# Optimization experiments

Hardware: AMD Instinct MI355X
Metric: run time of the kernel (lower is better)

The kernel has to match this reference:

```python
import jax, jax.numpy as jnp
import numpy as np

B, T, IN = 4, 1024, 172
D, H, FF, L, NCLS = 512, 8, 2048, 8, 1296
HD = D // H
EPS = 1e-5


def setup_inputs() -> dict:
    key = jax.random.key(0)
    ks = jax.random.split(key, 16)
    rn = lambda k, s, sc=0.02: jax.random.normal(k, s, jnp.float32) * sc
    return {
        "poses": jax.random.normal(ks[0], (B, T, IN), jnp.float32),
        "pose_w": rn(ks[1], (D, IN)), "pose_b": jnp.zeros((D,), jnp.float32),
        "in_w": rn(ks[2], (L, 3 * D, D)), "in_b": jnp.zeros((L, 3 * D), jnp.float32),
        "out_w": rn(ks[3], (L, D, D)), "out_b": jnp.zeros((L, D), jnp.float32),
        "ln1_g": jnp.ones((L, D), jnp.float32), "ln1_b": jnp.zeros((L, D), jnp.float32),
        "ffn_w1": rn(ks[4], (L, FF, D)), "ffn_b1": jnp.zeros((L, FF), jnp.float32),
        "ffn_w2": rn(ks[5], (L, D, FF)), "ffn_b2": jnp.zeros((L, D), jnp.float32),
        "ln2_g": jnp.ones((L, D), jnp.float32), "ln2_b": jnp.zeros((L, D), jnp.float32),
        "tcn1_w": rn(ks[6], (512, D, 5)), "tcn1_b": jnp.zeros((512,), jnp.float32),
        "tcn2_w": rn(ks[7], (D, 512, 5)), "tcn2_b": jnp.zeros((D,), jnp.float32),
        "fc1_w": rn(ks[8], (128, D)), "fc1_b": jnp.zeros((128,), jnp.float32),
        "fc2_w": rn(ks[9], (NCLS, 128)), "fc2_b": jnp.zeros((NCLS,), jnp.float32),
    }


def _pos_enc(seq_len, d):
    # PositionalEncoding1D: interleaved sin/cos per frequency pair
    inv_freq = 1.0 / (10000.0 ** (jnp.arange(0, d, 2, dtype=jnp.float32) / d))
    ang = jnp.arange(seq_len, dtype=jnp.float32)[:, None] * inv_freq  # [T, d/2]
    return jnp.stack([jnp.sin(ang), jnp.cos(ang)], axis=-1).reshape(seq_len, d)


def _ln(x, g, b):
    m = x.mean(-1, keepdims=True)
    v = jnp.var(x, axis=-1, keepdims=True)
    return (x - m) * jax.lax.rsqrt(v + EPS) * g + b


def _encoder_layer(x, iw, ib, ow, ob, g1, b1, w1, c1, w2, c2, g2, b2):
    # post-norm TransformerEncoderLayer, eager (non-flash) attention
    Bc, Tc, _ = x.shape
    qkv = x @ iw.T + ib                       # [B,T,3D]
    q, k, v = jnp.split(qkv, 3, axis=-1)
    q = q.reshape(Bc, Tc, H, HD)
    k = k.reshape(Bc, Tc, H, HD)
    v = v.reshape(Bc, Tc, H, HD)
    scores = jnp.einsum('bqhd,bkhd->bhqk', q, k) / jnp.sqrt(jnp.float32(HD))
    attn = jax.nn.softmax(scores, axis=-1)    # explicit weights (need_weights=True)
    o = jnp.einsum('bhqk,bkhd->bqhd', attn, v).reshape(Bc, Tc, D)
    o = o @ ow.T + ob
    x = _ln(x + o, g1, b1)
    f = jax.nn.relu(x @ w1.T + c1) @ w2.T + c2
    return _ln(x + f, g2, b2)


def _conv1d(x, w, b):  # x [B,T,C_in], w [C_out,C_in,5], pad=2
    y = jax.lax.conv_general_dilated(
        x.transpose(0, 2, 1), w, window_strides=(1,), padding=((2, 2),),
        dimension_numbers=('NCH', 'OIH', 'NCH'))
    return y.transpose(0, 2, 1) + b


def _avgpool2(x):  # kernel=2 stride=2 along time
    Bc, Tc, C = x.shape
    return x.reshape(Bc, Tc // 2, 2, C).mean(axis=2)


def reference(poses, pose_w, pose_b, in_w, in_b, out_w, out_b, ln1_g, ln1_b,
              ffn_w1, ffn_b1, ffn_w2, ffn_b2, ln2_g, ln2_b,
              tcn1_w, tcn1_b, tcn2_w, tcn2_b, fc1_w, fc1_b, fc2_w, fc2_b):
    x = poses.reshape(poses.shape[0], poses.shape[1], -1) @ pose_w.T + pose_b
    x = x + _pos_enc(x.shape[1], D)[None]

    def run_stack(h, idx):
        for i in idx:
            h = _encoder_layer(h, in_w[i], in_b[i], out_w[i], out_b[i],
                               ln1_g[i], ln1_b[i], ffn_w1[i], ffn_b1[i],
                               ffn_w2[i], ffn_b2[i], ln2_g[i], ln2_b[i])
        return h

    h = run_stack(x, (0, 1))
    h = run_stack(h, (2, 3)) + h
    h = run_stack(h, (4, 5)) + h
    h = run_stack(h, (6, 7)) + h

    h = _avgpool2(h)                 # [B,T/2,D]
    h = _conv1d(h, tcn1_w, tcn1_b)   # [B,T/2,512]
    h = _avgpool2(h)                 # [B,T/4,512]
    h = _conv1d(h, tcn2_w, tcn2_b)   # [B,T/4,D]
    h = h @ fc1_w.T + fc1_b
    logits = h @ fc2_w.T + fc2_b     # [B,T/4,num_classes]
    return logits
```

## Files before the change

kernel.cpp:

```cpp
#include <hip/hip_runtime.h>
#include <hip/hip_bf16.h>

static constexpr int kB = 4;
static constexpr int kT = 1024;
static constexpr int kIn = 172;
static constexpr int kD = 512;
static constexpr int kH = 8;
static constexpr int kHD = 64;
static constexpr int kFF = 2048;
static constexpr int kNCLS = 1296;
static constexpr float kEps = 1e-5f;

typedef __attribute__((ext_vector_type(8))) short bf16x8_t;
typedef __attribute__((ext_vector_type(4))) float f32x4_t;
typedef __attribute__((ext_vector_type(8))) unsigned short u16x8_t;
typedef __attribute__((ext_vector_type(4))) unsigned short u16x4_t;

static __device__ __forceinline__ unsigned short f2bf(float f) {
  unsigned int u = __float_as_uint(f);
  unsigned int r = (u + 0x7fffu + ((u >> 16) & 1u)) >> 16;
  return (unsigned short)r;
}

__global__ void cvt_kernel(const float* __restrict__ src, ushort* __restrict__ dst, int n8)
{
  const int i = blockIdx.x * 256 + threadIdx.x;
  if (i >= n8) return;
  const float4 a = *(const float4*)&src[i * 8];
  const float4 b = *(const float4*)&src[i * 8 + 4];
  u16x8_t t;
  t[0] = f2bf(a.x); t[1] = f2bf(a.y); t[2] = f2bf(a.z); t[3] = f2bf(a.w);
  t[4] = f2bf(b.x); t[5] = f2bf(b.y); t[6] = f2bf(b.z); t[7] = f2bf(b.w);
  *(u16x8_t*)&dst[i * 8] = t;
}

template<int MR, int NR>
__global__ __launch_bounds__(256) void bgemm_kernel(
    const ushort* __restrict__ A, const ushort* __restrict__ W,
    const float* __restrict__ bias, const float* __restrict__ resid,
    float* __restrict__ C, ushort* __restrict__ Cb, int M, int N, int K, int doRelu)
{
  constexpr int BM = MR * 32, BN = NR * 32, BK = 32;
  constexpr int AI = BM / 64;
  constexpr int BI = BN / 64;
  __shared__ ushort As[BM * BK];
  __shared__ ushort Bs[BN * BK];

  const int tid = threadIdx.x;
  int bid = blockIdx.y * gridDim.x + blockIdx.x;
  const int nwg = gridDim.x * gridDim.y;
  if ((nwg & 7) == 0) bid = (bid & 7) * (nwg >> 3) + (bid >> 3);
  const int bm = (bid / gridDim.x) * BM, bn = (bid % gridDim.x) * BN;

  const int wv = tid >> 6, lane = tid & 63;
  const int lr = lane & 15, lg = lane >> 4;
  const int wr = wv >> 1, wc = wv & 1;

  const int arow0 = wv * (BM / 4);
  const int brow0 = wv * (BN / 4);
  const int lrow = lane >> 2;
  const int lchunk = (lane & 3) * 8;

  f32x4_t acc[MR][NR];
#pragma unroll
  for (int m = 0; m < MR; ++m)
#pragma unroll
    for (int n = 0; n < NR; ++n) acc[m][n] = (f32x4_t){0.f, 0.f, 0.f, 0.f};

  auto stage = [&](int k0) {
#pragma unroll
    for (int i = 0; i < AI; ++i) {
      const ushort* g = A + (size_t)(bm + arow0 + i * 16 + lrow) * K + k0 + lchunk;
      __builtin_amdgcn_global_load_lds(
          (const __attribute__((address_space(1))) void*)g,
          (__attribute__((address_space(3))) void*)&As[(arow0 + i * 16) * BK], 16, 0, 0);
    }
#pragma unroll
    for (int i = 0; i < BI; ++i) {
      const ushort* g = W + (size_t)(bn + brow0 + i * 16 + lrow) * K + k0 + lchunk;
      __builtin_amdgcn_global_load_lds(
          (const __attribute__((address_space(1))) void*)g,
          (__attribute__((address_space(3))) void*)&Bs[(brow0 + i * 16) * BK], 16, 0, 0);
    }
  };

  stage(0);
  const int nsteps = K >> 5;
  for (int s = 0; s < nsteps; ++s) {
    __syncthreads();
    bf16x8_t af[MR], bf[NR];
#pragma unroll
    for (int m = 0; m < MR; ++m)
      af[m] = *(const bf16x8_t*)&As[(wr * MR * 16 + m * 16 + lr) * BK + lg * 8];
#pragma unroll
    for (int n = 0; n < NR; ++n)
      bf[n] = *(const bf16x8_t*)&Bs[(wc * NR * 16 + n * 16 + lr) * BK + lg * 8];
#pragma unroll
    for (int n = 0; n < NR; ++n)
#pragma unroll
      for (int m = 0; m < MR; ++m)
        acc[m][n] = __builtin_amdgcn_mfma_f32_16x16x32_bf16(af[m], bf[n], acc[m][n], 0, 0, 0);
    __syncthreads();
    if (s + 1 < nsteps) stage((s + 1) << 5);
  }

#pragma unroll
  for (int m = 0; m < MR; ++m) {
#pragma unroll
    for (int v = 0; v < 4; ++v) {
      const int mm = bm + wr * MR * 16 + m * 16 + lg * 4 + v;
#pragma unroll
      for (int n = 0; n < NR; ++n) {
        const int nn = bn + wc * NR * 16 + n * 16 + lr;
        float val = acc[m][n][v] + bias[nn];
        if (doRelu) val = fmaxf(val, 0.f);
        if (resid) val += resid[(size_t)mm * N + nn];
        if (C)  C[(size_t)mm * N + nn] = val;
        if (Cb) Cb[(size_t)mm * N + nn] = f2bf(val);
      }
    }
  }
}

#define GBM 64
#define GBN 64
#define GBK 16
#define LDST 68

__global__ __launch_bounds__(256) void gemm_kernel(
    const float* __restrict__ A, const float* __restrict__ W,
    const float* __restrict__ bias, const float* __restrict__ resid,
    float* __restrict__ C, int M, int N, int K, int doRelu)
{
  __shared__ __align__(16) float As[GBK][LDST];
  __shared__ __align__(16) float Ws[GBK][LDST];
  const int tid = threadIdx.x;
  const int bm = blockIdx.y * GBM;
  const int bn = blockIdx.x * GBN;
  const int tx = tid & 15, ty = tid >> 4;
  const int li = tid >> 2;
  const int lk = (tid & 3) << 2;

  float acc[4][4];
#pragma unroll
  for (int i = 0; i < 4; ++i)
#pragma unroll
    for (int j = 0; j < 4; ++j) acc[i][j] = 0.f;

  for (int k0 = 0; k0 < K; k0 += GBK) {
    float4 av = make_float4(0.f, 0.f, 0.f, 0.f);
    float4 wv = make_float4(0.f, 0.f, 0.f, 0.f);
    {
      const int m = bm + li;
      if (m < M) {
        if (k0 + lk + 4 <= K) {
          av = *(const float4*)&A[(size_t)m * K + k0 + lk];
        } else {
          float t4[4] = {0.f, 0.f, 0.f, 0.f};
          for (int c = 0; c < 4; ++c) { int k = k0 + lk + c; if (k < K) t4[c] = A[(size_t)m * K + k]; }
          av = make_float4(t4[0], t4[1], t4[2], t4[3]);
        }
      }
      const int n = bn + li;
      if (n < N) {
        if (k0 + lk + 4 <= K) {
          wv = *(const float4*)&W[(size_t)n * K + k0 + lk];
        } else {
          float t4[4] = {0.f, 0.f, 0.f, 0.f};
          for (int c = 0; c < 4; ++c) { int k = k0 + lk + c; if (k < K) t4[c] = W[(size_t)n * K + k]; }
          wv = make_float4(t4[0], t4[1], t4[2], t4[3]);
        }
      }
    }
    __syncthreads();
    As[lk + 0][li] = av.x; As[lk + 1][li] = av.y; As[lk + 2][li] = av.z; As[lk + 3][li] = av.w;
    Ws[lk + 0][li] = wv.x; Ws[lk + 1][li] = wv.y; Ws[lk + 2][li] = wv.z; Ws[lk + 3][li] = wv.w;
    __syncthreads();
#pragma unroll
    for (int kk = 0; kk < GBK; ++kk) {
      const float4 a4 = *(const float4*)&As[kk][ty << 2];
      const float4 b4 = *(const float4*)&Ws[kk][tx << 2];
      const float a[4] = {a4.x, a4.y, a4.z, a4.w};
      const float b[4] = {b4.x, b4.y, b4.z, b4.w};
#pragma unroll
      for (int i = 0; i < 4; ++i)
#pragma unroll
        for (int j = 0; j < 4; ++j) acc[i][j] = fmaf(a[i], b[j], acc[i][j]);
    }
  }

#pragma unroll
  for (int i = 0; i < 4; ++i) {
    const int m = bm + (ty << 2) + i;
    if (m >= M) continue;
#pragma unroll
    for (int j = 0; j < 4; ++j) {
      const int n = bn + (tx << 2) + j;
      if (n >= N) continue;
      float v = acc[i][j] + bias[n];
      if (doRelu) v = fmaxf(v, 0.f);
      if (resid) v += resid[(size_t)m * N + n];
      C[(size_t)m * N + n] = v;
    }
  }
}

__global__ __launch_bounds__(256) void ln_kernel(
    float* __restrict__ X, ushort* __restrict__ Xb,
    const float* __restrict__ g, const float* __restrict__ bta,
    const float* Padd, float* Pout)
{
  const int row = blockIdx.x;
  const int tid = threadIdx.x;
  float* xr = X + (size_t)row * kD;
  const float x0 = xr[tid];
  const float x1 = xr[tid + 256];
  float s = x0 + x1;
  float q = x0 * x0 + x1 * x1;
#pragma unroll
  for (int off = 32; off > 0; off >>= 1) {
    s += __shfl_down(s, off);
    q += __shfl_down(q, off);
  }
  __shared__ float ss[4], qq[4];
  const int w = tid >> 6;
  if ((tid & 63) == 0) { ss[w] = s; qq[w] = q; }
  __syncthreads();
  const float S = ss[0] + ss[1] + ss[2] + ss[3];
  const float Q = qq[0] + qq[1] + qq[2] + qq[3];
  const float mean = S * (1.f / kD);
  const float var = Q * (1.f / kD) - mean * mean;
  const float inv = rsqrtf(var + kEps);
  float v0 = (x0 - mean) * inv * g[tid] + bta[tid];
  float v1 = (x1 - mean) * inv * g[tid + 256] + bta[tid + 256];
  if (Padd) {
    v0 += Padd[(size_t)row * kD + tid];
    v1 += Padd[(size_t)row * kD + tid + 256];
  }
  xr[tid] = v0; xr[tid + 256] = v1;
  ushort* xb = Xb + (size_t)row * kD;
  xb[tid] = f2bf(v0); xb[tid + 256] = f2bf(v1);
  if (Pout) {
    Pout[(size_t)row * kD + tid] = v0;
    Pout[(size_t)row * kD + tid + 256] = v1;
  }
}

#define KSTR 72
#define PSTR 74
__global__ __launch_bounds__(256) void attn_mfma_kernel(
    const ushort* __restrict__ qkv, ushort* __restrict__ O)
{
  const int b = blockIdx.z, h = blockIdx.y;
  const int q0 = blockIdx.x << 6;
  const int tid = threadIdx.x;
  const int wv = tid >> 6, lane = tid & 63;
  const int lr = lane & 15;
  const int lg = lane >> 4;

  __shared__ ushort Ks[64 * KSTR];
  __shared__ ushort Vt[64 * KSTR];
  __shared__ ushort Pl[4][16 * PSTR];

  bf16x8_t qa[2];
  {
    const ushort* qrow = qkv + ((size_t)(b * kT + q0 + wv * 16 + lr)) * (3 * kD) + h * kHD + lg * 8;
    qa[0] = *(const bf16x8_t*)qrow;
    qa[1] = *(const bf16x8_t*)(qrow + 32);
  }

  float m_[4], l_[4];
  f32x4_t oacc[4];
#pragma unroll
  for (int r = 0; r < 4; ++r) { m_[r] = -1e30f; l_[r] = 0.f; }
#pragma unroll
  for (int nb = 0; nb < 4; ++nb) oacc[nb] = (f32x4_t){0.f, 0.f, 0.f, 0.f};

  const int srow = tid >> 2;
  const int sd   = (tid & 3) << 4;
  const int vkp  = tid & 31;
  const int vdh  = tid >> 5;

  u16x8_t k0_, k1_, v0_, v1_;
  auto load_regs = [&](int kt) {
    const ushort* kr = qkv + ((size_t)(b * kT + (kt << 6) + srow)) * (3 * kD) + kD + h * kHD + sd;
    k0_ = *(const u16x8_t*)kr;
    k1_ = *(const u16x8_t*)(kr + 8);
    const ushort* vr = qkv + ((size_t)(b * kT + (kt << 6) + 2 * vkp)) * (3 * kD) + 2 * kD + h * kHD + vdh * 8;
    v0_ = *(const u16x8_t*)vr;
    v1_ = *(const u16x8_t*)(vr + 3 * kD);
  };

  load_regs(0);
  for (int kt = 0; kt < kT / 64; ++kt) {
    __syncthreads();
    {
      *(u16x8_t*)&Ks[srow * KSTR + sd]     = k0_;
      *(u16x8_t*)&Ks[srow * KSTR + sd + 8] = k1_;
#pragma unroll
      for (int e = 0; e < 8; ++e) {
        const unsigned int packv = (unsigned int)v0_[e] | ((unsigned int)v1_[e] << 16);
        *(unsigned int*)&Vt[(vdh * 8 + e) * KSTR + 2 * vkp] = packv;
      }
    }
    __syncthreads();
    if (kt + 1 < kT / 64) load_regs(kt + 1);

    f32x4_t s[4];
#pragma unroll
    for (int cc = 0; cc < 4; ++cc) {
      const ushort* kb = &Ks[(cc * 16 + lr) * KSTR + lg * 8];
      const bf16x8_t kf0 = *(const bf16x8_t*)kb;
      const bf16x8_t kf1 = *(const bf16x8_t*)(kb + 32);
      f32x4_t acc = (f32x4_t){0.f, 0.f, 0.f, 0.f};
      acc = __builtin_amdgcn_mfma_f32_16x16x32_bf16(qa[0], kf0, acc, 0, 0, 0);
      acc = __builtin_amdgcn_mfma_f32_16x16x32_bf16(qa[1], kf1, acc, 0, 0, 0);
#pragma unroll
      for (int r = 0; r < 4; ++r) acc[r] *= 0.125f;
      s[cc] = acc;
    }

#pragma unroll
    for (int r = 0; r < 4; ++r) {
      float mx = fmaxf(fmaxf(s[0][r], s[1][r]), fmaxf(s[2][r], s[3][r]));
      mx = fmaxf(mx, __shfl_xor(mx, 1));
      mx = fmaxf(mx, __shfl_xor(mx, 2));
      mx = fmaxf(mx, __shfl_xor(mx, 4));
      mx = fmaxf(mx, __shfl_xor(mx, 8));
      const float mnew = fmaxf(m_[r], mx);
      const float alpha = __expf(m_[r] - mnew);
      float sum = 0.f;
#pragma unroll
      for (int cc = 0; cc < 4; ++cc) {
        const float p = __expf(s[cc][r] - mnew);
        s[cc][r] = p;
        sum += p;
      }
      sum += __shfl_xor(sum, 1);
      sum += __shfl_xor(sum, 2);
      sum += __shfl_xor(sum, 4);
      sum += __shfl_xor(sum, 8);
      l_[r] = l_[r] * alpha + sum;
      m_[r] = mnew;
#pragma unroll
      for (int nb = 0; nb < 4; ++nb) oacc[nb][r] *= alpha;
#pragma unroll
      for (int cc = 0; cc < 4; ++cc)
        Pl[wv][(lg * 4 + r) * PSTR + cc * 16 + lr] = f2bf(s[cc][r]);
    }

    const bf16x8_t pa0 = *(const bf16x8_t*)&Pl[wv][lr * PSTR + lg * 8];
    const bf16x8_t pa1 = *(const bf16x8_t*)&Pl[wv][lr * PSTR + 32 + lg * 8];
#pragma unroll
    for (int nb = 0; nb < 4; ++nb) {
      const ushort* vb = &Vt[(nb * 16 + lr) * KSTR + lg * 8];
      const bf16x8_t vf0 = *(const bf16x8_t*)vb;
      const bf16x8_t vf1 = *(const bf16x8_t*)(vb + 32);
      oacc[nb] = __builtin_amdgcn_mfma_f32_16x16x32_bf16(pa0, vf0, oacc[nb], 0, 0, 0);
      oacc[nb] = __builtin_amdgcn_mfma_f32_16x16x32_bf16(pa1, vf1, oacc[nb], 0, 0, 0);
    }
  }

#pragma unroll
  for (int nb = 0; nb < 4; ++nb) {
#pragma unroll
    for (int r = 0; r < 4; ++r) {
      const int row = lg * 4 + r;
      const int col = nb * 16 + lr;
      O[((size_t)(b * kT + q0 + wv * 16 + row)) * kD + h * kHD + col] = f2bf(oacc[nb][r] / l_[r]);
    }
  }
}

__global__ __launch_bounds__(256) void posenc_kernel(float* __restrict__ X, ushort* __restrict__ Xb)
{
  const int bt = blockIdx.x;
  const int t = bt & (kT - 1);
  float* row = X + (size_t)bt * kD;
  ushort* rb = Xb + (size_t)bt * kD;
#pragma unroll
  for (int p = 0; p < 2; ++p) {
    const int d = threadIdx.x + p * 256;
    const int j = d >> 1;
    const float inv = expf(-(float)j * 0.03597789207803197f);
    const float ang = (float)t * inv;
    const float pe = (d & 1) ? cosf(ang) : sinf(ang);
    const float v = row[d] + pe;
    row[d] = v;
    rb[d] = f2bf(v);
  }
}

__global__ void im2col_pool_kernel(const float* __restrict__ X, ushort* __restrict__ X5,
                                   int Tt, int n4)
{
  const int idx = blockIdx.x * 256 + threadIdx.x;
  if (idx >= n4) return;
  const int ci4 = idx & 127;
  int r = idx >> 7;
  const int tap = r % 5; r /= 5;
  const int t = r % Tt;
  const int b = r / Tt;
  const int ts = t + tap - 2;
  u16x4_t o = (u16x4_t){0, 0, 0, 0};
  if (ts >= 0 && ts < Tt) {
    const float* p = X + ((size_t)(b * 2 * Tt + 2 * ts)) * kD + ci4 * 4;
    const float4 x0 = *(const float4*)p;
    const float4 x1 = *(const float4*)(p + kD);
    o[0] = f2bf(0.5f * (x0.x + x1.x)); o[1] = f2bf(0.5f * (x0.y + x1.y));
    o[2] = f2bf(0.5f * (x0.z + x1.z)); o[3] = f2bf(0.5f * (x0.w + x1.w));
  }
  *(u16x4_t*)&X5[((size_t)(b * Tt + t)) * 2560 + tap * kD + ci4 * 4] = o;
}

__global__ void convw_t_kernel(const float* __restrict__ w, ushort* __restrict__ Wt)
{
  const int idx = blockIdx.x * 256 + threadIdx.x;
  if (idx >= 512 * 512 * 5) return;
  const int ci = idx & 511;
  int r = idx >> 9;
  const int tap = r % 5;
  const int co = r / 5;
  Wt[(size_t)co * 2560 + tap * 512 + ci] = f2bf(w[(size_t)co * 2560 + ci * 5 + tap]);
}

extern "C" void kernel_launch(void* const* d_in, const int* in_sizes, int n_in,
                              void* d_out, int out_size, void* d_ws, size_t ws_size,
                              hipStream_t stream)
{
  (void)in_sizes; (void)n_in; (void)out_size;
  const float* poses  = (const float*)d_in[0];
  const float* pose_w = (const float*)d_in[1];
  const float* pose_b = (const float*)d_in[2];
  const float* in_w   = (const float*)d_in[3];
  const float* in_b   = (const float*)d_in[4];
  const float* out_w  = (const float*)d_in[5];
  const float* out_b  = (const float*)d_in[6];
  const float* ln1_g  = (const float*)d_in[7];
  const float* ln1_b  = (const float*)d_in[8];
  const float* ffn_w1 = (const float*)d_in[9];
  const float* ffn_b1 = (const float*)d_in[10];
  const float* ffn_w2 = (const float*)d_in[11];
  const float* ffn_b2 = (const float*)d_in[12];
  const float* ln2_g  = (const float*)d_in[13];
  const float* ln2_b  = (const float*)d_in[14];
  const float* tcn1_w = (const float*)d_in[15];
  const float* tcn1_b = (const float*)d_in[16];
  const float* tcn2_w = (const float*)d_in[17];
  const float* tcn2_b = (const float*)d_in[18];
  const float* fc1_w  = (const float*)d_in[19];
  const float* fc1_b  = (const float*)d_in[20];
  const float* fc2_w  = (const float*)d_in[21];
  const float* fc2_b  = (const float*)d_in[22];

  char* base = (char*)d_ws;
  float*  A    = (float*)(base);
  float*  Y    = (float*)(base + 8388608);
  float*  P    = (float*)(base + 16777216);
  ushort* Abf  = (ushort*)(base + 25165824);
  ushort* QKV  = (ushort*)(base + 29360128);
  ushort* Ybf  = QKV;
  ushort* X5   = QKV;
  ushort* MID  = (ushort*)(base + 41943040);
  ushort* ATTb = MID;
  ushort* CW   = MID;
  ushort* Wbf  = (ushort*)(base + 58720256);

  const size_t nWq = (size_t)3 * kD * kD;
  const size_t nWo = (size_t)kD * kD;
  const size_t nW1 = (size_t)kFF * kD;
  const size_t nW2 = (size_t)kD * kFF;
  const size_t nWl = nWq + nWo + nW1 + nW2;
  const bool fullW = ws_size >= (size_t)58720256 + nWl * 8 * 2;

  const int M = kB * kT;
  dim3 blk(256);
  auto cvt = [&](const float* s, ushort* d, size_t n) {
    cvt_kernel<<<(int)((n / 8 + 255) / 256), blk, 0, stream>>>(s, d, (int)(n / 8));
  };

  if (fullW) {
    cvt(in_w,   Wbf,                        nWq * 8);
    cvt(out_w,  Wbf + nWq * 8,              nWo * 8);
    cvt(ffn_w1, Wbf + nWq * 8 + nWo * 8,    nW1 * 8);
    cvt(ffn_w2, Wbf + (nWq + nWo + nW1) * 8, nW2 * 8);
  }

  gemm_kernel<<<dim3(kD / GBN, M / GBM), blk, 0, stream>>>(poses, pose_w, pose_b, nullptr, A, M, kD, kIn, 0);
  posenc_kernel<<<M, blk, 0, stream>>>(A, Abf);

  for (int l = 0; l < 8; ++l) {
    const ushort *Wq, *Wo, *W1, *W2;
    if (fullW) {
      Wq = Wbf + (size_t)l * nWq;
      Wo = Wbf + nWq * 8 + (size_t)l * nWo;
      W1 = Wbf + nWq * 8 + nWo * 8 + (size_t)l * nW1;
      W2 = Wbf + (nWq + nWo + nW1) * 8 + (size_t)l * nW2;
    } else {
      cvt(in_w   + (size_t)l * nWq, Wbf, nWq);
      cvt(out_w  + (size_t)l * nWo, Wbf + nWq, nWo);
      cvt(ffn_w1 + (size_t)l * nW1, Wbf + nWq + nWo, nW1);
      cvt(ffn_w2 + (size_t)l * nW2, Wbf + nWq + nWo + nW1, nW2);
      Wq = Wbf; Wo = Wbf + nWq; W1 = Wbf + nWq + nWo; W2 = Wbf + nWq + nWo + nW1;
    }

    bgemm_kernel<4, 4><<<dim3(3 * kD / 128, M / 128), blk, 0, stream>>>(
        Abf, Wq, in_b + (size_t)l * 3 * kD, nullptr, nullptr, QKV, M, 3 * kD, kD, 0);
    attn_mfma_kernel<<<dim3(kT / 64, kH, kB), blk, 0, stream>>>(QKV, ATTb);
    bgemm_kernel<4, 2><<<dim3(kD / 64, M / 128), blk, 0, stream>>>(
        ATTb, Wo, out_b + (size_t)l * kD, A, Y, nullptr, M, kD, kD, 0);
    ln_kernel<<<M, blk, 0, stream>>>(Y, Ybf, ln1_g + (size_t)l * kD, ln1_b + (size_t)l * kD,
                                     nullptr, nullptr);
    bgemm_kernel<4, 4><<<dim3(kFF / 128, M / 128), blk, 0, stream>>>(
        Ybf, W1, ffn_b1 + (size_t)l * kFF, nullptr, nullptr, MID, M, kFF, kD, 1);
    bgemm_kernel<4, 2><<<dim3(kD / 64, M / 128), blk, 0, stream>>>(
        MID, W2, ffn_b2 + (size_t)l * kD, Y, A, nullptr, M, kD, kFF, 0);
    {
      const float* padd = (l == 3 || l == 5 || l == 7) ? P : nullptr;
      float* pout = (l == 1 || l == 3 || l == 5) ? P : nullptr;
      ln_kernel<<<M, blk, 0, stream>>>(A, Abf, ln2_g + (size_t)l * kD, ln2_b + (size_t)l * kD,
                                       padd, pout);
    }
  }

  {
    const int T1 = kT / 2;
    const int T2 = kT / 4;
    convw_t_kernel<<<(512 * 512 * 5 + 255) / 256, blk, 0, stream>>>(tcn1_w, CW);
    const int n4a = kB * T1 * 5 * (kD / 4);
    im2col_pool_kernel<<<(n4a + 255) / 256, blk, 0, stream>>>(A, X5, T1, n4a);
    bgemm_kernel<4, 2><<<dim3(kD / 64, kB * T1 / 128), blk, 0, stream>>>(
        X5, CW, tcn1_b, nullptr, Y, nullptr, kB * T1, kD, 2560, 0);
    convw_t_kernel<<<(512 * 512 * 5 + 255) / 256, blk, 0, stream>>>(tcn2_w, CW);
    const int n4b = kB * T2 * 5 * (kD / 4);
    im2col_pool_kernel<<<(n4b + 255) / 256, blk, 0, stream>>>(Y, X5, T2, n4b);
    bgemm_kernel<4, 2><<<dim3(kD / 64, kB * T2 / 128), blk, 0, stream>>>(
        X5, CW, tcn2_b, nullptr, A, nullptr, kB * T2, kD, 2560, 0);
    const int Mh = kB * T2;
    gemm_kernel<<<dim3(128 / GBN, Mh / GBM), blk, 0, stream>>>(A, fc1_w, fc1_b, nullptr, Y, Mh, 128, kD, 0);
    gemm_kernel<<<dim3((kNCLS + GBN - 1) / GBN, Mh / GBM), blk, 0, stream>>>(
        Y, fc2_w, fc2_b, nullptr, (float*)d_out, Mh, kNCLS, 128, 0);
  }
}
```

Baseline: 1.561 ms.

## Restructure bf16 GEMM with register prefetch, BK=64 padded LDS and 512-thread blocks

The bf16 MFMA GEMM is reworked in three ways. It now prefetches the next K tile into registers while computing the current one, replacing the synchronous global_load_lds staging. It uses BK=64 with padded LDS rows (stride 72) to avoid bank conflicts, and blocks grow to 8 waves with configurable warp layout. The conv GEMMs also use smaller M tiles to get more blocks. This costs more registers and LDS per block, which may lower occupancy.

```diff
diff --git a/kernel.cpp b/kernel.cpp
--- a/kernel.cpp
+++ b/kernel.cpp
@@ -34,17 +34,19 @@
   *(u16x8_t*)&dst[i * 8] = t;
 }
 
-template<int MR, int NR>
-__global__ __launch_bounds__(256) void bgemm_kernel(
+template<int MR, int NR, int WM, int WN>
+__global__ __launch_bounds__(WM * WN * 64) void bgemm_kernel(
     const ushort* __restrict__ A, const ushort* __restrict__ W,
     const float* __restrict__ bias, const float* __restrict__ resid,
     float* __restrict__ C, ushort* __restrict__ Cb, int M, int N, int K, int doRelu)
 {
-  constexpr int BM = MR * 32, BN = NR * 32, BK = 32;
-  constexpr int AI = BM / 64;
-  constexpr int BI = BN / 64;
-  __shared__ ushort As[BM * BK];
-  __shared__ ushort Bs[BN * BK];
+  constexpr int THREADS = WM * WN * 64;
+  constexpr int BM = MR * 16 * WM, BN = NR * 16 * WN;
+  constexpr int SRD = 72;
+  constexpr int TPRA = THREADS / BM, CSA = 64 / TPRA, NLA = CSA / 8;
+  constexpr int TPRB = THREADS / BN, CSB = 64 / TPRB, NLB = CSB / 8;
+  __shared__ ushort As[BM * SRD];
+  __shared__ ushort Bs[BN * SRD];
 
   const int tid = threadIdx.x;
   int bid = blockIdx.y * gridDim.x + blockIdx.x;
@@ -54,12 +56,10 @@
 
   const int wv = tid >> 6, lane = tid & 63;
   const int lr = lane & 15, lg = lane >> 4;
-  const int wr = wv >> 1, wc = wv & 1;
-
-  const int arow0 = wv * (BM / 4);
-  const int brow0 = wv * (BN / 4);
-  const int lrow = lane >> 2;
-  const int lchunk = (lane & 3) * 8;
+  const int wr = wv / WN, wc = wv % WN;
+
+  const int ra = tid / TPRA, ca = (tid % TPRA) * CSA;
+  const int rb = tid / TPRB, cb = (tid % TPRB) * CSB;
 
   f32x4_t acc[MR][NR];
 #pragma unroll
@@ -67,41 +67,47 @@
 #pragma unroll
     for (int n = 0; n < NR; ++n) acc[m][n] = (f32x4_t){0.f, 0.f, 0.f, 0.f};
 
-  auto stage = [&](int k0) {
-#pragma unroll
-    for (int i = 0; i < AI; ++i) {
-      const ushort* g = A + (size_t)(bm + arow0 + i * 16 + lrow) * K + k0 + lchunk;
-      __builtin_amdgcn_global_load_lds(
-          (const __attribute__((address_space(1))) void*)g,
-          (__attribute__((address_space(3))) void*)&As[(arow0 + i * 16) * BK], 16, 0, 0);
-    }
-#pragma unroll
-    for (int i = 0; i < BI; ++i) {
-      const ushort* g = W + (size_t)(bn + brow0 + i * 16 + lrow) * K + k0 + lchunk;
-      __builtin_amdgcn_global_load_lds(
-          (const __attribute__((address_space(1))) void*)g,
-          (__attribute__((address_space(3))) void*)&Bs[(brow0 + i * 16) * BK], 16, 0, 0);
-    }
+  u16x8_t pa[NLA], pb[NLB];
+  auto loadAB = [&](int k0) {
+    const ushort* ap = A + (size_t)(bm + ra) * K + k0 + ca;
+#pragma unroll
+    for (int j = 0; j < NLA; ++j) pa[j] = *(const u16x8_t*)(ap + j * 8);
+    const ushort* bp = W + (size_t)(bn + rb) * K + k0 + cb;
+#pragma unroll
+    for (int j = 0; j < NLB; ++j) pb[j] = *(const u16x8_t*)(bp + j * 8);
   };
-
-  stage(0);
-  const int nsteps = K >> 5;
+  auto storeLDS = [&]() {
+#pragma unroll
+    for (int j = 0; j < NLA; ++j) *(u16x8_t*)&As[ra * SRD + ca + j * 8] = pa[j];
+#pragma unroll
+    for (int j = 0; j < NLB; ++j) *(u16x8_t*)&Bs[rb * SRD + cb + j * 8] = pb[j];
+  };
+
+  loadAB(0);
+  storeLDS();
+  __syncthreads();
+
+  const int nsteps = K >> 6;
   for (int s = 0; s < nsteps; ++s) {
+    const bool more = (s + 1) < nsteps;
+    if (more) loadAB((s + 1) << 6);
+
+#pragma unroll
+    for (int kk = 0; kk < 2; ++kk) {
+      bf16x8_t af[MR];
+#pragma unroll
+      for (int m = 0; m < MR; ++m)
+        af[m] = *(const bf16x8_t*)&As[(wr * MR * 16 + m * 16 + lr) * SRD + kk * 32 + lg * 8];
+#pragma unroll
+      for (int n = 0; n < NR; ++n) {
+        const bf16x8_t bf = *(const bf16x8_t*)&Bs[(wc * NR * 16 + n * 16 + lr) * SRD + kk * 32 + lg * 8];
+#pragma unroll
+        for (int m = 0; m < MR; ++m)
+          acc[m][n] = __builtin_amdgcn_mfma_f32_16x16x32_bf16(af[m], bf, acc[m][n], 0, 0, 0);
+      }
+    }
     __syncthreads();
-    bf16x8_t af[MR], bf[NR];
-#pragma unroll
-    for (int m = 0; m < MR; ++m)
-      af[m] = *(const bf16x8_t*)&As[(wr * MR * 16 + m * 16 + lr) * BK + lg * 8];
-#pragma unroll
-    for (int n = 0; n < NR; ++n)
-      bf[n] = *(const bf16x8_t*)&Bs[(wc * NR * 16 + n * 16 + lr) * BK + lg * 8];
-#pragma unroll
-    for (int n = 0; n < NR; ++n)
-#pragma unroll
-      for (int m = 0; m < MR; ++m)
-        acc[m][n] = __builtin_amdgcn_mfma_f32_16x16x32_bf16(af[m], bf[n], acc[m][n], 0, 0, 0);
-    __syncthreads();
-    if (s + 1 < nsteps) stage((s + 1) << 5);
+    if (more) { storeLDS(); __syncthreads(); }
   }
 
 #pragma unroll
@@ -475,6 +481,7 @@
 
   const int M = kB * kT;
   dim3 blk(256);
+  dim3 blk512(512);
   auto cvt = [&](const float* s, ushort* d, size_t n) {
     cvt_kernel<<<(int)((n / 8 + 255) / 256), blk, 0, stream>>>(s, d, (int)(n / 8));
   };
@@ -504,16 +511,16 @@
       Wq = Wbf; Wo = Wbf + nWq; W1 = Wbf + nWq + nWo; W2 = Wbf + nWq + nWo + nW1;
     }
 
-    bgemm_kernel<4, 4><<<dim3(3 * kD / 128, M / 128), blk, 0, stream>>>(
+    bgemm_kernel<4, 2, 2, 4><<<dim3(3 * kD / 128, M / 128), blk512, 0, stream>>>(
         Abf, Wq, in_b + (size_t)l * 3 * kD, nullptr, nullptr, QKV, M, 3 * kD, kD, 0);
     attn_mfma_kernel<<<dim3(kT / 64, kH, kB), blk, 0, stream>>>(QKV, ATTb);
-    bgemm_kernel<4, 2><<<dim3(kD / 64, M / 128), blk, 0, stream>>>(
+    bgemm_kernel<2, 2, 4, 2><<<dim3(kD / 64, M / 128), blk512, 0, stream>>>(
         ATTb, Wo, out_b + (size_t)l * kD, A, Y, nullptr, M, kD, kD, 0);
     ln_kernel<<<M, blk, 0, stream>>>(Y, Ybf, ln1_g + (size_t)l * kD, ln1_b + (size_t)l * kD,
                                      nullptr, nullptr);
-    bgemm_kernel<4, 4><<<dim3(kFF / 128, M / 128), blk, 0, stream>>>(
+    bgemm_kernel<4, 2, 2, 4><<<dim3(kFF / 128, M / 128), blk512, 0, stream>>>(
         Ybf, W1, ffn_b1 + (size_t)l * kFF, nullptr, nullptr, MID, M, kFF, kD, 1);
-    bgemm_kernel<4, 2><<<dim3(kD / 64, M / 128), blk, 0, stream>>>(
+    bgemm_kernel<2, 2, 4, 2><<<dim3(kD / 64, M / 128), blk512, 0, stream>>>(
         MID, W2, ffn_b2 + (size_t)l * kD, Y, A, nullptr, M, kD, kFF, 0);
     {
       const float* padd = (l == 3 || l == 5 || l == 7) ? P : nullptr;
@@ -529,12 +536,12 @@
     convw_t_kernel<<<(512 * 512 * 5 + 255) / 256, blk, 0, stream>>>(tcn1_w, CW);
     const int n4a = kB * T1 * 5 * (kD / 4);
     im2col_pool_kernel<<<(n4a + 255) / 256, blk, 0, stream>>>(A, X5, T1, n4a);
-    bgemm_kernel<4, 2><<<dim3(kD / 64, kB * T1 / 128), blk, 0, stream>>>(
+    bgemm_kernel<1, 2, 4, 2><<<dim3(kD / 64, kB * T1 / 64), blk512, 0, stream>>>(
         X5, CW, tcn1_b, nullptr, Y, nullptr, kB * T1, kD, 2560, 0);
     convw_t_kernel<<<(512 * 512 * 5 + 255) / 256, blk, 0, stream>>>(tcn2_w, CW);
     const int n4b = kB * T2 * 5 * (kD / 4);
     im2col_pool_kernel<<<(n4b + 255) / 256, blk, 0, stream>>>(Y, X5, T2, n4b);
-    bgemm_kernel<4, 2><<<dim3(kD / 64, kB * T2 / 128), blk, 0, stream>>>(
+    bgemm_kernel<1, 2, 4, 2><<<dim3(kD / 64, kB * T2 / 64), blk512, 0, stream>>>(
         X5, CW, tcn2_b, nullptr, A, nullptr, kB * T2, kD, 2560, 0);
     const int Mh = kB * T2;
     gemm_kernel<<<dim3(128 / GBN, Mh / GBM), blk, 0, stream>>>(A, fc1_w, fc1_b, nullptr, Y, Mh, 128, kD, 0);
```

New measurement: 1.281 ms. 1.22x faster.
